# Kernel tuning notes

Hardware: AMD Instinct MI355X
Metric: run time of the kernel (lower is better)

Reference implementation:

```python
import jax, jax.numpy as jnp
import numpy as np

# Module hyperparameters (from init_kwargs)
LATENT = 1024
H = 16          # num query heads
HK = 4          # num key/value heads (GQA)
D = 64          # head_dim
CAUSAL = True
QKV_OUT = (3 * H + 2 * HK) * D  # 3584, as defined in the source module


def setup_inputs() -> dict:
    key = jax.random.key(0)
    k1, k2, k3 = jax.random.split(key, 3)
    B, S = 2, 2048
    x = jax.random.normal(k1, (B, S, LATENT), dtype=jnp.float32)
    # nn.Linear weights are [out_features, in_features]; scale like torch default init
    w_qkv = jax.random.normal(k2, (QKV_OUT, LATENT), dtype=jnp.float32) / np.sqrt(LATENT)
    w_out = jax.random.normal(k3, (LATENT, H * D), dtype=jnp.float32) / np.sqrt(H * D)
    return {"x": x, "w_qkv": w_qkv, "w_out": w_out}


def reference(x, w_qkv, w_out):
    B, S, _ = x.shape
    scale = 1.0 / np.sqrt(D).astype(np.float32)

    # Fused QKV projection: [B,S,(3H+2HK)*D]
    qkv = jnp.einsum('bsl,ol->bso', x, w_qkv)

    # Split: q takes H heads, k and v take HK heads each (GQA).
    # (The extra 2*H*D columns of the fused projection are allocated by the
    #  source module but unused by q/k/v, matching its layer sizing.)
    q = qkv[..., : H * D].reshape(B, S, H, D)
    k = qkv[..., H * D:(H + HK) * D].reshape(B, S, HK, D)
    v = qkv[..., (H + HK) * D:(H + 2 * HK) * D].reshape(B, S, HK, D)

    # Expand KV heads to match query heads (group factor H // HK)
    rep = H // HK
    k = jnp.repeat(k, rep, axis=2)  # [B,S,H,D]
    v = jnp.repeat(v, rep, axis=2)

    # Scaled dot-product attention
    scores = jnp.einsum('bshd,bthd->bhst', q, k) * scale  # [B,H,S,S]
    if CAUSAL:
        causal_mask = jnp.tril(jnp.ones((S, S), dtype=bool))
        scores = jnp.where(causal_mask, scores, jnp.finfo(scores.dtype).min)
    attn = jax.nn.softmax(scores, axis=-1)
    out = jnp.einsum('bhst,bthd->bshd', attn, v).reshape(B, S, H * D)

    # Output projection back to latent_size
    return jnp.einsum('bso,lo->bsl', out, w_out)
```

## Files before the change

kernel.cpp:

```cpp
#include <hip/hip_runtime.h>
#include <hip/hip_bf16.h>
#include <math.h>

typedef __attribute__((ext_vector_type(8))) short bf16x8;
typedef __attribute__((ext_vector_type(4))) float f32x4;
typedef unsigned short u16;
typedef unsigned int   u32;

#define DEVINL __device__ __forceinline__

DEVINL u16 f2bf(float x) {
    u32 u = __float_as_uint(x);
    u += 0x7fffu + ((u >> 16) & 1u);
    return (u16)(u >> 16);
}

DEVINL void gl_lds16(const void* g, void* s) {
    __builtin_amdgcn_global_load_lds(
        (const __attribute__((address_space(1))) u32*)g,
        (__attribute__((address_space(3))) u32*)s,
        16, 0, 0);
}

DEVINL f32x4 mfma16(bf16x8 a, bf16x8 b, f32x4 c) {
    return __builtin_amdgcn_mfma_f32_16x16x32_bf16(a, b, c, 0, 0, 0);
}

__global__ void cvt3(const float* __restrict__ x, const float* __restrict__ wq,
                     const float* __restrict__ wo,
                     u16* __restrict__ xb, u16* __restrict__ wqb, u16* __restrict__ wob) {
    int i = blockIdx.x * 256 + threadIdx.x;
    const float* s; u16* d; int j;
    if (i < 1048576)      { s = x;  d = xb;  j = i; }
    else if (i < 1441792) { s = wq; d = wqb; j = i - 1048576; }
    else                  { s = wo; d = wob; j = i - 1441792; }
    float4 v = ((const float4*)s)[j];
    ushort4 o;
    o.x = f2bf(v.x); o.y = f2bf(v.y); o.z = f2bf(v.z); o.w = f2bf(v.w);
    ((ushort4*)d)[j] = o;
}

template<int BN, int EP>
__launch_bounds__(256)
__global__ void gemm_rp(const u16* __restrict__ A, const u16* __restrict__ B,
                        const int N, const int K,
                        float* __restrict__ Cf,
                        u16* __restrict__ Qo, u16* __restrict__ Ko, u16* __restrict__ Vo)
{
    constexpr int NB = BN / 32;
    __shared__ __align__(16) u16 As[2][64 * 64];
    __shared__ __align__(16) u16 Bs[2][BN * 64];
    const int tid  = threadIdx.x;
    const int lane = tid & 63;
    const int quad = lane >> 4;
    const int lcol = lane & 15;
    const int w    = tid >> 6;
    const int wr   = w >> 1, wc = w & 1;
    const int lr   = lane >> 3;
    const int lc   = lane & 7;
    const int swst = lc ^ lr;
    const int rk   = lcol & 7;
    const int m0 = blockIdx.y * 64;
    const int n0 = blockIdx.x * BN;

    f32x4 acc[2][NB];
    for (int mb = 0; mb < 2; mb++)
        for (int nb = 0; nb < NB; nb++)
            for (int i = 0; i < 4; i++) acc[mb][nb][i] = 0.f;

    const u16* Ap = A + (m0 + w * 16 + lr) * K + swst * 8;
    const u16* Bp = B + (n0 + w * (BN / 4) + lr) * K + swst * 8;

    bf16x8 areg[2], breg[NB];
    for (int j = 0; j < 2; j++)  areg[j] = *(const bf16x8*)(Ap + j * 8 * K);
    for (int g = 0; g < NB; g++) breg[g] = *(const bf16x8*)(Bp + g * 8 * K);
    for (int j = 0; j < 2; j++)
        *(bf16x8*)&As[0][(w * 16 + j * 8 + lr) * 64 + lc * 8] = areg[j];
    for (int g = 0; g < NB; g++)
        *(bf16x8*)&Bs[0][(w * (BN / 4) + g * 8 + lr) * 64 + lc * 8] = breg[g];
    __syncthreads();

    int cur = 0;
    for (int k0 = 0; k0 < K; k0 += 64) {
        const bool more = (k0 + 64 < K);
        if (more) {
            for (int j = 0; j < 2; j++)  areg[j] = *(const bf16x8*)(Ap + j * 8 * K + k0 + 64);
            for (int g = 0; g < NB; g++) breg[g] = *(const bf16x8*)(Bp + g * 8 * K + k0 + 64);
        }
        bf16x8 af[2][2], bfv[NB][2];
        for (int ks = 0; ks < 2; ks++) {
            const int ch = ((ks * 4 + quad) ^ rk) * 8;
            for (int mb = 0; mb < 2; mb++)
                af[mb][ks] = *(const bf16x8*)&As[cur][(wr * 32 + mb * 16 + lcol) * 64 + ch];
            for (int nb = 0; nb < NB; nb++)
                bfv[nb][ks] = *(const bf16x8*)&Bs[cur][(wc * (BN / 2) + nb * 16 + lcol) * 64 + ch];
        }
        for (int ks = 0; ks < 2; ks++)
            for (int mb = 0; mb < 2; mb++)
                for (int nb = 0; nb < NB; nb++)
                    acc[mb][nb] = mfma16(af[mb][ks], bfv[nb][ks], acc[mb][nb]);
        if (more) {
            for (int j = 0; j < 2; j++)
                *(bf16x8*)&As[cur ^ 1][(w * 16 + j * 8 + lr) * 64 + lc * 8] = areg[j];
            for (int g = 0; g < NB; g++)
                *(bf16x8*)&Bs[cur ^ 1][(w * (BN / 4) + g * 8 + lr) * 64 + lc * 8] = breg[g];
        }
        __syncthreads();
        cur ^= 1;
    }

    if (EP == 0) {
        for (int mb = 0; mb < 2; mb++)
            for (int nb = 0; nb < NB; nb++) {
                int row = m0 + wr * 32 + mb * 16 + quad * 4;
                int col = n0 + wc * (BN / 2) + nb * 16 + lcol;
                for (int i = 0; i < 4; i++)
                    Cf[(row + i) * N + col] = acc[mb][nb][i];
            }
    } else {
        const float qsc = 0.18033688011112042f;
        for (int mb = 0; mb < 2; mb++)
            for (int nb = 0; nb < NB; nb++)
                for (int i = 0; i < 4; i++) {
                    int row = m0 + wr * 32 + mb * 16 + quad * 4 + i;
                    int col = n0 + wc * (BN / 2) + nb * 16 + lcol;
                    int bb = row >> 11, ss = row & 2047;
                    if (col < 1024) {
                        int hh = col >> 6, dd = col & 63;
                        Qo[((bb * 16 + hh) * 2048 + ss) * 64 + dd] = f2bf(acc[mb][nb][i] * qsc);
                    } else if (col < 1280) {
                        int c = col - 1024, hh = c >> 6, dd = c & 63;
                        Ko[((bb * 4 + hh) * 2048 + ss) * 64 + dd] = f2bf(acc[mb][nb][i]);
                    } else {
                        int c = col - 1280, hh = c >> 6, dd = c & 63;
                        Vo[((bb * 4 + hh) * 64 + dd) * 2048 + ss] = f2bf(acc[mb][nb][i]);
                    }
                }
    }
}

__launch_bounds__(256)
__global__ void attn_kernel(const u16* __restrict__ Qg, const u16* __restrict__ Kg,
                            const u16* __restrict__ Vtg, u16* __restrict__ Og)
{
    __shared__ __align__(16) u16 Ks[2][64 * 64];
    __shared__ __align__(16) u16 Vs[2][64 * 64];
    __shared__ __align__(16) u16 Ps[64 * 64];

    const int tid  = threadIdx.x;
    const int lane = tid & 63;
    const int w    = tid >> 6;
    const int quad = lane >> 4;
    const int lcol = lane & 15;
    const int lr   = lane >> 3;
    const int lc   = lane & 7;
    const int swst = lc ^ lr;
    const int rk   = lcol & 7;

    const int p  = blockIdx.x;
    const int h  = blockIdx.y;
    const int b  = blockIdx.z;
    const int hk = h >> 2;

    const u16* Qp = Qg  + (b * 16 + h) * 2048 * 64;
    const u16* Kp = Kg  + (b * 4 + hk) * 2048 * 64;
    const u16* Vp = Vtg + (b * 4 + hk) * 64 * 2048;

    for (int pass = 0; pass < 2; pass++) {
        const int qi = pass ? (31 - p) : p;
        const int q0 = qi * 64;
        const int nt = qi + 1;

        bf16x8 aqr[2];
        for (int ks = 0; ks < 2; ks++)
            aqr[ks] = *(const bf16x8*)(Qp + (q0 + w * 16 + lcol) * 64 + ks * 32 + quad * 8);

        for (int j = 0; j < 2; j++) {
            const int r = w * 16 + j * 8 + lr;
            gl_lds16(Kp + r * 64 + swst * 8,   &Ks[0][w * 1024 + j * 512]);
            gl_lds16(Vp + r * 2048 + swst * 8, &Vs[0][w * 1024 + j * 512]);
        }

        f32x4 o[4];
        float l_p[4];
        for (int db = 0; db < 4; db++)
            for (int i = 0; i < 4; i++) o[db][i] = 0.f;
        for (int i = 0; i < 4; i++) l_p[i] = 0.f;

        __syncthreads();

        for (int ti = 0; ti < nt; ti++) {
            const int cur = ti & 1;
            if (ti + 1 < nt) {
                const int nb = cur ^ 1;
                const int t0n = (ti + 1) * 64;
                for (int j = 0; j < 2; j++) {
                    const int r = w * 16 + j * 8 + lr;
                    gl_lds16(Kp + (t0n + r) * 64 + swst * 8, &Ks[nb][w * 1024 + j * 512]);
                    gl_lds16(Vp + r * 2048 + t0n + swst * 8, &Vs[nb][w * 1024 + j * 512]);
                }
            }

            f32x4 s[4];
            for (int cb = 0; cb < 4; cb++)
                for (int i = 0; i < 4; i++) s[cb][i] = 0.f;
            for (int ks = 0; ks < 2; ks++) {
                const int chq = ((ks * 4 + quad) ^ rk) * 8;
                for (int cb = 0; cb < 4; cb++) {
                    bf16x8 bk = *(const bf16x8*)&Ks[cur][(cb * 16 + lcol) * 64 + chq];
                    s[cb] = mfma16(aqr[ks], bk, s[cb]);
                }
            }

            if (ti == nt - 1) {
                for (int cb = 0; cb < 4; cb++)
                    for (int i = 0; i < 4; i++) {
                        const bool masked = (cb * 16 + lcol) > (w * 16 + quad * 4 + i);
                        s[cb][i] = masked ? -INFINITY : s[cb][i];
                    }
            }

            for (int cb = 0; cb < 4; cb++)
                for (int i = 0; i < 4; i++) {
                    const float pv = exp2f(s[cb][i]);
                    s[cb][i] = pv;
                    l_p[i] += pv;
                }

            for (int cb = 0; cb < 4; cb++)
                for (int i = 0; i < 4; i++) {
                    const int rl = quad * 4 + i;
                    const int cc = cb * 2 + (lcol >> 3);
                    Ps[(w * 16 + rl) * 64 + ((cc ^ (rl & 7)) << 3) + lc] =
                        (u16)(__float_as_uint(s[cb][i]) >> 16);
                }

            for (int kt = 0; kt < 2; kt++) {
                const int chp = ((kt * 4 + quad) ^ rk) * 8;
                bf16x8 ap = *(const bf16x8*)&Ps[(w * 16 + lcol) * 64 + chp];
                for (int db = 0; db < 4; db++) {
                    bf16x8 bv = *(const bf16x8*)&Vs[cur][(db * 16 + lcol) * 64 + chp];
                    o[db] = mfma16(ap, bv, o[db]);
                }
            }
            __syncthreads();
        }

        for (int i = 0; i < 4; i++) {
            float l = l_p[i];
            for (int x = 1; x < 16; x <<= 1) l += __shfl_xor(l, x);
            const float inv = 1.0f / l;
            const int srow = q0 + w * 16 + quad * 4 + i;
            for (int db = 0; db < 4; db++)
                Og[(b * 2048 + srow) * 1024 + h * 64 + db * 16 + lcol] = f2bf(o[db][i] * inv);
        }
    }
}

extern "C" void kernel_launch(void* const* d_in, const int* in_sizes, int n_in,
                              void* d_out, int out_size, void* d_ws, size_t ws_size,
                              hipStream_t stream) {
    const float* x     = (const float*)d_in[0];
    const float* w_qkv = (const float*)d_in[1];
    const float* w_out = (const float*)d_in[2];
    float* out = (float*)d_out;
    char* ws = (char*)d_ws;

    u16* xb  = (u16*)(ws);
    u16* wqb = (u16*)(ws + 8  * 1024 * 1024);
    u16* wob = (u16*)(ws + 11 * 1024 * 1024);
    u16* qb  = (u16*)(ws + 13 * 1024 * 1024);
    u16* kb  = (u16*)(ws + 21 * 1024 * 1024);
    u16* vtb = (u16*)(ws + 23 * 1024 * 1024);
    u16* aob = (u16*)(ws);

    cvt3<<<6656, 256, 0, stream>>>(x, w_qkv, w_out, xb, wqb, wob);

    gemm_rp<128, 1><<<dim3(12, 64), 256, 0, stream>>>(xb, wqb, 1536, 1024,
                                                      nullptr, qb, kb, vtb);
    attn_kernel<<<dim3(16, 16, 2), 256, 0, stream>>>(qb, kb, vtb, aob);
    gemm_rp<64, 0><<<dim3(16, 64), 256, 0, stream>>>(aob, wob, 1024, 1024,
                                                     out, nullptr, nullptr, nullptr);
}
```

Measured before the change: 170.3 us.

## Split attention KV tiles across two wave groups per block and merge

The attention block grows to 512 threads and splits into two 4-wave groups. Each group processes alternating KV tiles with its own double-buffered K/V/P LDS. The partial outputs and row sums are merged through LDS at the end, a split-K over the key dimension, and exp2f becomes the hardware exp2 builtin. This halves the sequential KV loop per block to raise parallelism, at the cost of doubled LDS, an extra reduction with barriers, and shared barriers that stall both groups on odd tile counts.

```diff
diff --git a/kernel.cpp b/kernel.cpp
--- a/kernel.cpp
+++ b/kernel.cpp
@@ -139,23 +139,26 @@
     }
 }
 
-__launch_bounds__(256)
+__launch_bounds__(512, 4)
 __global__ void attn_kernel(const u16* __restrict__ Qg, const u16* __restrict__ Kg,
                             const u16* __restrict__ Vtg, u16* __restrict__ Og)
 {
-    __shared__ __align__(16) u16 Ks[2][64 * 64];
-    __shared__ __align__(16) u16 Vs[2][64 * 64];
-    __shared__ __align__(16) u16 Ps[64 * 64];
+    __shared__ __align__(16) u16 Ks[2][2][64 * 64];
+    __shared__ __align__(16) u16 Vs[2][2][64 * 64];
+    __shared__ __align__(16) u16 Ps[2][64 * 64];
 
     const int tid  = threadIdx.x;
     const int lane = tid & 63;
-    const int w    = tid >> 6;
+    const int w8   = tid >> 6;
+    const int gpp  = w8 >> 2;
+    const int wg   = w8 & 3;
     const int quad = lane >> 4;
     const int lcol = lane & 15;
     const int lr   = lane >> 3;
     const int lc   = lane & 7;
     const int swst = lc ^ lr;
     const int rk   = lcol & 7;
+    const int hl   = lcol >> 3;
 
     const int p  = blockIdx.x;
     const int h  = blockIdx.y;
@@ -166,19 +169,27 @@
     const u16* Kp = Kg  + (b * 4 + hk) * 2048 * 64;
     const u16* Vp = Vtg + (b * 4 + hk) * 64 * 2048;
 
+    const int p0 = (wg * 16 + quad * 4) * 64 + ((hl ^ ((quad & 1) << 2)) << 3) + lc;
+
+    float* Ob = (float*)(&Ks[1][0][0]);
+    float* Lb = (float*)(&Vs[1][0][0]);
+
     for (int pass = 0; pass < 2; pass++) {
         const int qi = pass ? (31 - p) : p;
         const int q0 = qi * 64;
         const int nt = qi + 1;
+        const int nIter = (nt + 1) >> 1;
 
         bf16x8 aqr[2];
         for (int ks = 0; ks < 2; ks++)
-            aqr[ks] = *(const bf16x8*)(Qp + (q0 + w * 16 + lcol) * 64 + ks * 32 + quad * 8);
-
-        for (int j = 0; j < 2; j++) {
-            const int r = w * 16 + j * 8 + lr;
-            gl_lds16(Kp + r * 64 + swst * 8,   &Ks[0][w * 1024 + j * 512]);
-            gl_lds16(Vp + r * 2048 + swst * 8, &Vs[0][w * 1024 + j * 512]);
+            aqr[ks] = *(const bf16x8*)(Qp + (q0 + wg * 16 + lcol) * 64 + ks * 32 + quad * 8);
+
+        if (gpp < nt) {
+            for (int j = 0; j < 2; j++) {
+                const int r = wg * 16 + j * 8 + lr;
+                gl_lds16(Kp + (gpp * 64 + r) * 64 + swst * 8, &Ks[gpp][0][wg * 1024 + j * 512]);
+                gl_lds16(Vp + r * 2048 + gpp * 64 + swst * 8, &Vs[gpp][0][wg * 1024 + j * 512]);
+            }
         }
 
         f32x4 o[4];
@@ -189,71 +200,89 @@
 
         __syncthreads();
 
-        for (int ti = 0; ti < nt; ti++) {
-            const int cur = ti & 1;
-            if (ti + 1 < nt) {
-                const int nb = cur ^ 1;
-                const int t0n = (ti + 1) * 64;
+        for (int it = 0; it < nIter; ++it) {
+            const int cur = it & 1;
+            const int ti  = 2 * it + gpp;
+            const int tin = ti + 2;
+            if (tin < nt) {
+                const int nbuf = cur ^ 1;
                 for (int j = 0; j < 2; j++) {
-                    const int r = w * 16 + j * 8 + lr;
-                    gl_lds16(Kp + (t0n + r) * 64 + swst * 8, &Ks[nb][w * 1024 + j * 512]);
-                    gl_lds16(Vp + r * 2048 + t0n + swst * 8, &Vs[nb][w * 1024 + j * 512]);
-                }
-            }
-
-            f32x4 s[4];
-            for (int cb = 0; cb < 4; cb++)
-                for (int i = 0; i < 4; i++) s[cb][i] = 0.f;
-            for (int ks = 0; ks < 2; ks++) {
-                const int chq = ((ks * 4 + quad) ^ rk) * 8;
-                for (int cb = 0; cb < 4; cb++) {
-                    bf16x8 bk = *(const bf16x8*)&Ks[cur][(cb * 16 + lcol) * 64 + chq];
-                    s[cb] = mfma16(aqr[ks], bk, s[cb]);
-                }
-            }
-
-            if (ti == nt - 1) {
+                    const int r = wg * 16 + j * 8 + lr;
+                    gl_lds16(Kp + (tin * 64 + r) * 64 + swst * 8, &Ks[gpp][nbuf][wg * 1024 + j * 512]);
+                    gl_lds16(Vp + r * 2048 + tin * 64 + swst * 8, &Vs[gpp][nbuf][wg * 1024 + j * 512]);
+                }
+            }
+            if (ti < nt) {
+                f32x4 s[4];
+                for (int cb = 0; cb < 4; cb++)
+                    for (int i = 0; i < 4; i++) s[cb][i] = 0.f;
+                for (int ks = 0; ks < 2; ks++) {
+                    const int chq = ((ks * 4 + quad) ^ rk) * 8;
+                    for (int cb = 0; cb < 4; cb++) {
+                        bf16x8 bk = *(const bf16x8*)&Ks[gpp][cur][(cb * 16 + lcol) * 64 + chq];
+                        s[cb] = mfma16(aqr[ks], bk, s[cb]);
+                    }
+                }
+
+                if (ti == nt - 1) {
+                    for (int cb = 0; cb < 4; cb++)
+                        for (int i = 0; i < 4; i++) {
+                            const bool masked = (cb * 16 + lcol) > (wg * 16 + quad * 4 + i);
+                            s[cb][i] = masked ? -INFINITY : s[cb][i];
+                        }
+                }
+
                 for (int cb = 0; cb < 4; cb++)
                     for (int i = 0; i < 4; i++) {
-                        const bool masked = (cb * 16 + lcol) > (w * 16 + quad * 4 + i);
-                        s[cb][i] = masked ? -INFINITY : s[cb][i];
+                        const float pv = __builtin_amdgcn_exp2f(s[cb][i]);
+                        s[cb][i] = pv;
+                        l_p[i] += pv;
                     }
-            }
-
-            for (int cb = 0; cb < 4; cb++)
-                for (int i = 0; i < 4; i++) {
-                    const float pv = exp2f(s[cb][i]);
-                    s[cb][i] = pv;
-                    l_p[i] += pv;
-                }
-
-            for (int cb = 0; cb < 4; cb++)
-                for (int i = 0; i < 4; i++) {
-                    const int rl = quad * 4 + i;
-                    const int cc = cb * 2 + (lcol >> 3);
-                    Ps[(w * 16 + rl) * 64 + ((cc ^ (rl & 7)) << 3) + lc] =
-                        (u16)(__float_as_uint(s[cb][i]) >> 16);
-                }
-
-            for (int kt = 0; kt < 2; kt++) {
-                const int chp = ((kt * 4 + quad) ^ rk) * 8;
-                bf16x8 ap = *(const bf16x8*)&Ps[(w * 16 + lcol) * 64 + chp];
-                for (int db = 0; db < 4; db++) {
-                    bf16x8 bv = *(const bf16x8*)&Vs[cur][(db * 16 + lcol) * 64 + chp];
-                    o[db] = mfma16(ap, bv, o[db]);
+
+                for (int cb = 0; cb < 4; cb++)
+                    for (int i = 0; i < 4; i++)
+                        Ps[gpp][(p0 + i * 64) ^ (((cb * 2) ^ i) << 3)] =
+                            (u16)(__float_as_uint(s[cb][i]) >> 16);
+
+                for (int kt = 0; kt < 2; kt++) {
+                    const int chp = ((kt * 4 + quad) ^ rk) * 8;
+                    bf16x8 ap = *(const bf16x8*)&Ps[gpp][(wg * 16 + lcol) * 64 + chp];
+                    for (int db = 0; db < 4; db++) {
+                        bf16x8 bv = *(const bf16x8*)&Vs[gpp][cur][(db * 16 + lcol) * 64 + chp];
+                        o[db] = mfma16(ap, bv, o[db]);
+                    }
                 }
             }
             __syncthreads();
         }
 
+        float lrow[4];
         for (int i = 0; i < 4; i++) {
             float l = l_p[i];
             for (int x = 1; x < 16; x <<= 1) l += __shfl_xor(l, x);
-            const float inv = 1.0f / l;
-            const int srow = q0 + w * 16 + quad * 4 + i;
-            for (int db = 0; db < 4; db++)
-                Og[(b * 2048 + srow) * 1024 + h * 64 + db * 16 + lcol] = f2bf(o[db][i] * inv);
-        }
+            lrow[i] = l;
+        }
+        if (gpp == 1) {
+            for (int i = 0; i < 4; i++) {
+                const int row = wg * 16 + quad * 4 + i;
+                for (int db = 0; db < 4; db++)
+                    Ob[row * 64 + db * 16 + lcol] = o[db][i];
+                if (lcol == 0) Lb[row] = lrow[i];
+            }
+        }
+        __syncthreads();
+        if (gpp == 0) {
+            for (int i = 0; i < 4; i++) {
+                const int row = wg * 16 + quad * 4 + i;
+                const float inv = 1.0f / (lrow[i] + Lb[row]);
+                const int srow = q0 + row;
+                for (int db = 0; db < 4; db++) {
+                    const float val = (o[db][i] + Ob[row * 64 + db * 16 + lcol]) * inv;
+                    Og[(b * 2048 + srow) * 1024 + h * 64 + db * 16 + lcol] = f2bf(val);
+                }
+            }
+        }
+        __syncthreads();
     }
 }
 
@@ -278,7 +307,7 @@
 
     gemm_rp<128, 1><<<dim3(12, 64), 256, 0, stream>>>(xb, wqb, 1536, 1024,
                                                       nullptr, qb, kb, vtb);
-    attn_kernel<<<dim3(16, 16, 2), 256, 0, stream>>>(qb, kb, vtb, aob);
+    attn_kernel<<<dim3(16, 16, 2), 512, 0, stream>>>(qb, kb, vtb, aob);
     gemm_rp<64, 0><<<dim3(16, 64), 256, 0, stream>>>(aob, wob, 1024, 1024,
                                                      out, nullptr, nullptr, nullptr);
 }
```

Measured after the change: 156.6 us. 1.09x faster.
